# Optimization experiments

Hardware: AMD Instinct MI355X
Metric: run time of the kernel (lower is better)

## Reference

```python
import jax, jax.numpy as jnp
import numpy as np

GRID_SIZE = 5
SPLINE_ORDER = 3
KH, KW = 3, 3
STRIDE, PAD, DIL = 1, 1, 1


def make_grid(in_features, dtype=jnp.float32):
    # uniform grid over [-1, 1], extended by spline_order on each side
    h = 2.0 / GRID_SIZE
    g = jnp.arange(-SPLINE_ORDER, GRID_SIZE + SPLINE_ORDER + 1, dtype=dtype) * h - 1.0
    return jnp.broadcast_to(g, (in_features, g.shape[0]))  # (in, G)


def b_splines(x, grid):
    # x: (N, in); grid: (in, G). Cox-de Boor recursion.
    xg = x[..., None]  # (N, in, 1)
    bases = ((xg >= grid[:, :-1]) & (xg < grid[:, 1:])).astype(x.dtype)  # (N, in, G-1)
    for k in range(1, SPLINE_ORDER + 1):
        left = (xg - grid[:, : -(k + 1)]) / (grid[:, k:-1] - grid[:, : -(k + 1)])
        right = (grid[:, k + 1:] - xg) / (grid[:, k + 1:] - grid[:, 1:-k])
        bases = left * bases[..., :-1] + right * bases[..., 1:]
    return bases  # (N, in, grid_size + spline_order)


def setup_inputs() -> dict:
    key = jax.random.key(0)
    k1, k2, k3, k4 = jax.random.split(key, 4)
    B, C, H, W = 4, 64, 64, 64
    out_ch = 128
    patch_dim = C * KH * KW  # 576
    nbasis = GRID_SIZE + SPLINE_ORDER  # 8
    x = jax.random.normal(k1, (B, C, H, W), dtype=jnp.float32)
    base_weight = jax.random.normal(k2, (out_ch, patch_dim), dtype=jnp.float32) * 0.05
    spline_weight = jax.random.normal(k3, (out_ch, patch_dim, nbasis), dtype=jnp.float32) * 0.05
    spline_scaler = jax.random.normal(k4, (out_ch, patch_dim), dtype=jnp.float32) * 0.1 + 1.0
    return {"x": x, "base_weight": base_weight, "spline_weight": spline_weight, "spline_scaler": spline_scaler}


def reference(x, base_weight, spline_weight, spline_scaler):
    B, C, H, W = x.shape
    out_ch, patch_dim = base_weight.shape
    # im2col: (B, C*KH*KW, Ho, Wo), feature dim ordered (C, kh, kw) like F.unfold
    patches = jax.lax.conv_general_dilated_patches(
        x, filter_shape=(KH, KW), window_strides=(STRIDE, STRIDE),
        padding=((PAD, PAD), (PAD, PAD)), rhs_dilation=(DIL, DIL),
        dimension_numbers=("NCHW", "OIHW", "NCHW"))
    Ho = (H + 2 * PAD - DIL * (KH - 1) - 1) // STRIDE + 1
    Wo = (W + 2 * PAD - DIL * (KW - 1) - 1) // STRIDE + 1
    L = Ho * Wo
    p = patches.reshape(B, patch_dim, L).transpose(0, 2, 1).reshape(B * L, patch_dim)  # (N, D)
    grid = make_grid(patch_dim, p.dtype)
    base_out = jax.nn.silu(p) @ base_weight.T  # (N, out)
    bases = b_splines(p, grid)  # (N, D, nbasis)
    scaled_w = spline_weight * spline_scaler[..., None]  # (out, D, nbasis)
    spline_out = jnp.einsum("ndk,odk->no", bases, scaled_w)
    out = (base_out + spline_out).reshape(B, L, out_ch).transpose(0, 2, 1).reshape(B, out_ch, Ho, Wo)
    return out
```

## Files before the change

### kernel.cpp

```cpp
#include <hip/hip_runtime.h>
#include <hip/hip_bf16.h>

#define B_      4
#define C_IN    64
#define H_      64
#define W_      64
#define OUT_CH  128
#define HP_     66
#define CF      576
#define WP_BYTES  (9 * OUT_CH * CF * 2)
#define F_BYTES   (B_ * HP_ * HP_ * CF * 2)
#define P_OFFSET  (WP_BYTES + F_BYTES)

typedef __bf16 bf16x8 __attribute__((ext_vector_type(8)));
typedef float  f32x4  __attribute__((ext_vector_type(4)));
typedef _Float16 half8 __attribute__((ext_vector_type(8)));

__device__ __forceinline__ void compute_features(float x, float f[9]) {
    f[0] = x / (1.0f + __expf(-x));
    float g[12];
#pragma unroll
    for (int i = 0; i < 12; ++i) g[i] = (float)(i - 3) * 0.4f - 1.0f;
    float bb[11];
#pragma unroll
    for (int i = 0; i < 11; ++i) bb[i] = (x >= g[i] && x < g[i + 1]) ? 1.0f : 0.0f;
#pragma unroll
    for (int i = 0; i < 10; ++i)
        bb[i] = (x - g[i]) * (1.0f / (g[i + 1] - g[i])) * bb[i]
              + (g[i + 2] - x) * (1.0f / (g[i + 2] - g[i + 1])) * bb[i + 1];
#pragma unroll
    for (int i = 0; i < 9; ++i)
        bb[i] = (x - g[i]) * (1.0f / (g[i + 2] - g[i])) * bb[i]
              + (g[i + 3] - x) * (1.0f / (g[i + 3] - g[i + 1])) * bb[i + 1];
#pragma unroll
    for (int i = 0; i < 8; ++i)
        bb[i] = (x - g[i]) * (1.0f / (g[i + 3] - g[i])) * bb[i]
              + (g[i + 4] - x) * (1.0f / (g[i + 4] - g[i + 1])) * bb[i + 1];
#pragma unroll
    for (int i = 0; i < 8; ++i) f[1 + i] = bb[i];
}

__global__ __launch_bounds__(256) void prep_kernel(
        const float* __restrict__ x, __hip_bfloat16* __restrict__ F,
        const float* __restrict__ bw, const float* __restrict__ sw,
        const float* __restrict__ sc, __hip_bfloat16* __restrict__ Wp) {
    __shared__ float xs[64][33];
    int blk = blockIdx.x;
    int tid = threadIdx.x;

    if (blk >= 528) {
        int idx = (blk - 528) * 256 + tid;
        if (idx < 589824) {
            int o = idx / 4608;
            int r = idx - o * 4608;
            int d = r >> 3;
            int j = r & 7;
            int tap = d % 9;
            int c   = d / 9;
            float v = sw[idx] * sc[o * 576 + d];
            Wp[(tap * OUT_CH + o) * CF + (j + 1) * 64 + c] = __float2bfloat16(v);
        } else {
            int k = idx - 589824;
            int o = k / 576;
            int d = k - o * 576;
            int tap = d % 9;
            int c   = d / 9;
            Wp[(tap * OUT_CH + o) * CF + c] = __float2bfloat16(bw[k]);
        }
        return;
    }

    int half = blk & 1;
    int bh   = blk >> 1;
    int b  = bh / HP_;
    int hp = bh % HP_;
    int h  = hp - 1;

    float f0[9];
    compute_features(0.0f, f0);

    bool interior_row = (h >= 0) && (h < H_);
    if (interior_row) {
        int wl = tid & 31;
        int c8 = tid >> 5;
#pragma unroll
        for (int i = 0; i < 8; ++i) {
            int c = c8 * 8 + i;
            xs[c][wl] = x[((b * C_IN + c) * H_ + h) * W_ + half * 32 + wl];
        }
    }
    __syncthreads();

    int c  = tid & 63;
    int wg = tid >> 6;
    __hip_bfloat16* Frow = F + (size_t)((b * HP_ + hp) * HP_) * CF;

    if (!interior_row) {
        for (int wp = half * 33 + wg; wp < half * 33 + 33; wp += 4) {
            __hip_bfloat16* dst = Frow + (size_t)wp * CF + c;
#pragma unroll
            for (int j = 0; j < 9; ++j) dst[j * 64] = __float2bfloat16(f0[j]);
        }
        return;
    }
    if (half == 0 && wg == 0) {
        __hip_bfloat16* dst = Frow + c;
#pragma unroll
        for (int j = 0; j < 9; ++j) dst[j * 64] = __float2bfloat16(f0[j]);
    }
    if (half == 1 && wg == 3) {
        __hip_bfloat16* dst = Frow + (size_t)65 * CF + c;
#pragma unroll
        for (int j = 0; j < 9; ++j) dst[j * 64] = __float2bfloat16(f0[j]);
    }
    for (int w2l = wg; w2l < 32; w2l += 4) {
        float xv = xs[c][w2l];
        float f[9];
        compute_features(xv, f);
        int wp = half * 32 + w2l + 1;
        __hip_bfloat16* dst = Frow + (size_t)wp * CF + c;
#pragma unroll
        for (int j = 0; j < 9; ++j) dst[j * 64] = __float2bfloat16(f[j]);
    }
}

__global__ __launch_bounds__(256, 2) void gemm_kernel(
        const __hip_bfloat16* __restrict__ Fb, const __hip_bfloat16* __restrict__ Wpb,
        _Float16* __restrict__ P) {
    __shared__ __align__(16) ushort As[2][8192];
    __shared__ __align__(16) ushort Bs[2][8192];

    const ushort* F  = (const ushort*)Fb;
    const ushort* Wp = (const ushort*)Wpb;

    int tid  = threadIdx.x;
    int lane = tid & 63;
    int w    = tid >> 6;
    int l15  = lane & 15;
    int lq   = lane >> 4;
    int wm = w & 1;
    int wn = w >> 1;
    int srow = lane >> 3;
    int sl7  = lane & 7;
    int c8s  = sl7 ^ srow;

    int hwb = blockIdx.x;
    int l   = ((hwb & 7) << 6) | (hwb >> 3);
    int q   = l >> 6;
    int r   = l & 63;
    int b   = q >> 1;
    int g   = ((q & 1) << 1) | (r >> 5);
    int ho0 = (r & 31) << 1;
    int c0 = (g == 0) ? 0 : (21 + 20 * (g - 1));
    int c1 = c0 + ((g == 0) ? 21 : 20);

    f32x4 acc[4][4];
#pragma unroll
    for (int i = 0; i < 4; ++i)
#pragma unroll
        for (int j = 0; j < 4; ++j) acc[i][j] = (f32x4){0.f, 0.f, 0.f, 0.f};

    auto prefetch = [&](int ch, int buf) {
        int tap = ch / 9;
        int kc  = ch - tap * 9;
        int kh  = tap / 3;
        int kw  = tap - kh * 3;
#pragma unroll
        for (int rr = 0; rr < 4; ++rr) {
            int row = (rr * 4 + w) * 8 + srow;
            int hp = ho0 + (row >> 6) + kh;
            int wp = (row & 63) + kw;
            const ushort* srcA = F + (size_t)((b * HP_ + hp) * HP_ + wp) * CF
                                   + kc * 64 + c8s * 8;
            __builtin_amdgcn_global_load_lds(
                (const __attribute__((address_space(1))) unsigned int*)srcA,
                (__attribute__((address_space(3))) unsigned int*)&As[buf][(rr * 4 + w) * 512],
                16, 0, 0);
            const ushort* srcB = Wp + (size_t)(tap * OUT_CH + row) * CF
                                    + kc * 64 + c8s * 8;
            __builtin_amdgcn_global_load_lds(
                (const __attribute__((address_space(1))) unsigned int*)srcB,
                (__attribute__((address_space(3))) unsigned int*)&Bs[buf][(rr * 4 + w) * 512],
                16, 0, 0);
        }
    };

    int buf = 0;
    prefetch(c0, 0);
    prefetch(c0 + 1, 1);
    for (int ch = c0; ch < c1; ++ch) {
        if (ch + 1 < c1) asm volatile("s_waitcnt vmcnt(8)\n\ts_barrier" ::: "memory");
        else             asm volatile("s_waitcnt vmcnt(0)\n\ts_barrier" ::: "memory");

        bf16x8 af[2][4], bq[2][4];
#pragma unroll
        for (int ks = 0; ks < 2; ++ks) {
#pragma unroll
            for (int mt = 0; mt < 4; ++mt) {
                int o  = wm * 64 + mt * 16 + l15;
                int sl = o * 8 + ((ks * 4 + lq) ^ (o & 7));
                af[ks][mt] = *(const bf16x8*)&Bs[buf][sl * 8];
            }
#pragma unroll
            for (int nt = 0; nt < 4; ++nt) {
                int p  = wn * 64 + nt * 16 + l15;
                int sl = p * 8 + ((ks * 4 + lq) ^ (p & 7));
                bq[ks][nt] = *(const bf16x8*)&As[buf][sl * 8];
            }
        }
        asm volatile("s_waitcnt lgkmcnt(0)\n\ts_barrier" ::: "memory");
        if (ch + 2 < c1) prefetch(ch + 2, buf);

        __builtin_amdgcn_s_setprio(1);
#pragma unroll
        for (int ks = 0; ks < 2; ++ks)
#pragma unroll
            for (int mt = 0; mt < 4; ++mt)
#pragma unroll
                for (int nt = 0; nt < 4; ++nt)
                    acc[mt][nt] = __builtin_amdgcn_mfma_f32_16x16x32_bf16(
                        af[ks][mt], bq[ks][nt], acc[mt][nt], 0, 0, 0);
        __builtin_amdgcn_s_setprio(0);
        buf ^= 1;
    }

    _Float16* Pg = P + ((size_t)(g * 4 + b) * OUT_CH) * 4096 + ho0 * 64;
#pragma unroll
    for (int mt = 0; mt < 4; ++mt) {
        int o = wm * 64 + mt * 16 + lq * 4;
#pragma unroll
        for (int nt = 0; nt < 4; ++nt) {
            int pix = wn * 64 + nt * 16 + l15;
            _Float16* dst = Pg + (size_t)o * 4096 + pix;
#pragma unroll
            for (int rr = 0; rr < 4; ++rr)
                dst[(size_t)rr * 4096] = (_Float16)acc[mt][nt][rr];
        }
    }
}

__global__ __launch_bounds__(256) void reduce_kernel(
        const half8* __restrict__ P, float4* __restrict__ out) {
    const int GS = 262144;
    int i = blockIdx.x * 256 + threadIdx.x;
    half8 a = P[i], bb = P[GS + i], c = P[2 * GS + i], d = P[3 * GS + i];
    float4 o0, o1;
#pragma unroll
    for (int j = 0; j < 4; ++j)
        ((float*)&o0)[j] = (float)a[j] + (float)bb[j] + (float)c[j] + (float)d[j];
#pragma unroll
    for (int j = 0; j < 4; ++j)
        ((float*)&o1)[j] = (float)a[4 + j] + (float)bb[4 + j] + (float)c[4 + j] + (float)d[4 + j];
    out[i * 2]     = o0;
    out[i * 2 + 1] = o1;
}

extern "C" void kernel_launch(void* const* d_in, const int* in_sizes, int n_in,
                              void* d_out, int out_size, void* d_ws, size_t ws_size,
                              hipStream_t stream) {
    const float* x  = (const float*)d_in[0];
    const float* bw = (const float*)d_in[1];
    const float* sw = (const float*)d_in[2];
    const float* sc = (const float*)d_in[3];
    float* out = (float*)d_out;

    __hip_bfloat16* Wp = (__hip_bfloat16*)d_ws;
    __hip_bfloat16* F  = (__hip_bfloat16*)((char*)d_ws + WP_BYTES);
    _Float16*       P  = (_Float16*)((char*)d_ws + P_OFFSET);

    prep_kernel<<<528 + 2592, 256, 0, stream>>>(x, F, bw, sw, sc, Wp);
    gemm_kernel<<<512, 256, 0, stream>>>(F, Wp, P);
    reduce_kernel<<<1024, 256, 0, stream>>>((const half8*)P, (float4*)out);
}
```

Before: 107.0 us.

## Fuse split-K reduction into GEMM epilogue via atomic last-block counter

Removes the separate reduce kernel. Each GEMM block bumps a per-tile atomic counter after writing its fp16 partial, and the fourth block to arrive sums the four partials and writes the fp32 output. The counters are zeroed by an extra block in the prep kernel. The block-to-tile mapping also changes so the four channel groups of one tile run in separate waves, which affects L2 locality and adds fence and atomic overhead.

```diff
diff --git a/kernel.cpp b/kernel.cpp
--- a/kernel.cpp
+++ b/kernel.cpp
@@ -11,6 +11,7 @@
 #define WP_BYTES  (9 * OUT_CH * CF * 2)
 #define F_BYTES   (B_ * HP_ * HP_ * CF * 2)
 #define P_OFFSET  (WP_BYTES + F_BYTES)
+#define CTR_OFFSET (P_OFFSET + 16777216)
 
 typedef __bf16 bf16x8 __attribute__((ext_vector_type(8)));
 typedef float  f32x4  __attribute__((ext_vector_type(4)));
@@ -43,10 +44,16 @@
 __global__ __launch_bounds__(256) void prep_kernel(
         const float* __restrict__ x, __hip_bfloat16* __restrict__ F,
         const float* __restrict__ bw, const float* __restrict__ sw,
-        const float* __restrict__ sc, __hip_bfloat16* __restrict__ Wp) {
+        const float* __restrict__ sc, __hip_bfloat16* __restrict__ Wp,
+        int* __restrict__ ctr) {
     __shared__ float xs[64][33];
     int blk = blockIdx.x;
     int tid = threadIdx.x;
+
+    if (blk >= 3120) {
+        if (tid < 128) ctr[tid] = 0;
+        return;
+    }
 
     if (blk >= 528) {
         int idx = (blk - 528) * 256 + tid;
@@ -126,9 +133,10 @@
 
 __global__ __launch_bounds__(256, 2) void gemm_kernel(
         const __hip_bfloat16* __restrict__ Fb, const __hip_bfloat16* __restrict__ Wpb,
-        _Float16* __restrict__ P) {
+        _Float16* __restrict__ P, float* __restrict__ out, int* __restrict__ ctr) {
     __shared__ __align__(16) ushort As[2][8192];
     __shared__ __align__(16) ushort Bs[2][8192];
+    __shared__ int lastflag;
 
     const ushort* F  = (const ushort*)Fb;
     const ushort* Wp = (const ushort*)Wpb;
@@ -144,13 +152,11 @@
     int sl7  = lane & 7;
     int c8s  = sl7 ^ srow;
 
-    int hwb = blockIdx.x;
-    int l   = ((hwb & 7) << 6) | (hwb >> 3);
-    int q   = l >> 6;
-    int r   = l & 63;
-    int b   = q >> 1;
-    int g   = ((q & 1) << 1) | (r >> 5);
-    int ho0 = (r & 31) << 1;
+    int blk = blockIdx.x;
+    int g   = blk >> 7;
+    int t   = blk & 127;
+    int b   = t >> 5;
+    int ho0 = (t & 31) << 1;
     int c0 = (g == 0) ? 0 : (21 + 20 * (g - 1));
     int c1 = c0 + ((g == 0) ? 21 : 20);
 
@@ -237,22 +243,35 @@
                 dst[(size_t)rr * 4096] = (_Float16)acc[mt][nt][rr];
         }
     }
-}
-
-__global__ __launch_bounds__(256) void reduce_kernel(
-        const half8* __restrict__ P, float4* __restrict__ out) {
-    const int GS = 262144;
-    int i = blockIdx.x * 256 + threadIdx.x;
-    half8 a = P[i], bb = P[GS + i], c = P[2 * GS + i], d = P[3 * GS + i];
-    float4 o0, o1;
-#pragma unroll
-    for (int j = 0; j < 4; ++j)
-        ((float*)&o0)[j] = (float)a[j] + (float)bb[j] + (float)c[j] + (float)d[j];
-#pragma unroll
-    for (int j = 0; j < 4; ++j)
-        ((float*)&o1)[j] = (float)a[4 + j] + (float)bb[4 + j] + (float)c[4 + j] + (float)d[4 + j];
-    out[i * 2]     = o0;
-    out[i * 2 + 1] = o1;
+
+    __threadfence();
+    if (tid == 0)
+        lastflag = (atomicAdd(&ctr[t], 1) == 3);
+    __syncthreads();
+    if (!lastflag) return;
+    __threadfence();
+
+    const half8* Ph = (const half8*)P;
+    for (int k = 0; k < 8; ++k) {
+        int hh  = tid + k * 256;
+        int o   = hh >> 4;
+        int col = (hh & 15) * 8;
+        size_t off0 = ((size_t)b * OUT_CH + o) * 4096 + ho0 * 64 + col;
+        half8 a0 = Ph[(off0 + (size_t)0 * 4 * OUT_CH * 4096) >> 3];
+        half8 a1 = Ph[(off0 + (size_t)1 * 4 * OUT_CH * 4096) >> 3];
+        half8 a2 = Ph[(off0 + (size_t)2 * 4 * OUT_CH * 4096) >> 3];
+        half8 a3 = Ph[(off0 + (size_t)3 * 4 * OUT_CH * 4096) >> 3];
+        float4 o0, o1;
+#pragma unroll
+        for (int j = 0; j < 4; ++j)
+            ((float*)&o0)[j] = (float)a0[j] + (float)a1[j] + (float)a2[j] + (float)a3[j];
+#pragma unroll
+        for (int j = 0; j < 4; ++j)
+            ((float*)&o1)[j] = (float)a0[4 + j] + (float)a1[4 + j] + (float)a2[4 + j] + (float)a3[4 + j];
+        float* dst = out + off0;
+        *(float4*)dst       = o0;
+        *(float4*)(dst + 4) = o1;
+    }
 }
 
 extern "C" void kernel_launch(void* const* d_in, const int* in_sizes, int n_in,
@@ -267,8 +286,8 @@
     __hip_bfloat16* Wp = (__hip_bfloat16*)d_ws;
     __hip_bfloat16* F  = (__hip_bfloat16*)((char*)d_ws + WP_BYTES);
     _Float16*       P  = (_Float16*)((char*)d_ws + P_OFFSET);
-
-    prep_kernel<<<528 + 2592, 256, 0, stream>>>(x, F, bw, sw, sc, Wp);
-    gemm_kernel<<<512, 256, 0, stream>>>(F, Wp, P);
-    reduce_kernel<<<1024, 256, 0, stream>>>((const half8*)P, (float4*)out);
-}
+    int*            ctr = (int*)((char*)d_ws + CTR_OFFSET);
+
+    prep_kernel<<<3121, 256, 0, stream>>>(x, F, bw, sw, sc, Wp, ctr);
+    gemm_kernel<<<512, 256, 0, stream>>>(F, Wp, P, out, ctr);
+}
```

After: 186.2 us. +74.0%, slower.
